# Optimization experiments

Hardware: AMD Instinct MI355X
Metric: run time of the kernel (lower is better)

## Reference

```python
import jax, jax.numpy as jnp
import numpy as np

B, S, D, H, K = 2, 2048, 1024, 16, 16


def setup_inputs() -> dict:
    key = jax.random.key(0)
    ks = jax.random.split(key, 8)
    s = 0.02
    def w(k, shape):
        return s * jax.random.normal(k, shape, jnp.float32)
    return {
        "x": jax.random.normal(ks[0], (B, S, D), jnp.float32),
        "Wq": w(ks[1], (D, D)), "bq": jnp.zeros((D,), jnp.float32),
        "Wk": w(ks[2], (D, D)), "bk": jnp.zeros((D,), jnp.float32),
        "Wv": w(ks[3], (D, D)), "bv": jnp.zeros((D,), jnp.float32),
        "Wo": w(ks[4], (D, D)), "bo": jnp.zeros((D,), jnp.float32),
        "Ws1": w(ks[5], (D, D // 2)), "bs1": jnp.zeros((D // 2,), jnp.float32),
        "Ws2": w(ks[6], (D // 2, 1)), "bs2": jnp.zeros((1,), jnp.float32),
    }


def reference(x, Wq, bq, Wk, bk, Wv, bv, Wo, bo, Ws1, bs1, Ws2, bs2):
    Bx, Sx, Dx = x.shape
    Dh = Dx // H
    # QKV projections -> [B, H, S, Dh]
    q = (x @ Wq + bq).reshape(Bx, Sx, H, Dh).transpose(0, 2, 1, 3)
    k = (x @ Wk + bk).reshape(Bx, Sx, H, Dh).transpose(0, 2, 1, 3)
    v = (x @ Wv + bv).reshape(Bx, Sx, H, Dh).transpose(0, 2, 1, 3)
    scores = jnp.einsum('bhqd,bhkd->bhqk', q, k) / np.float32(np.sqrt(Dh))
    # Lightning-indexer importance: [B, S]; identical across heads, so compute once.
    imp = jax.nn.sigmoid(jax.nn.relu(x @ Ws1 + bs1) @ Ws2 + bs2)[..., 0]
    _, idx = jax.lax.top_k(imp, K)  # [B, K]
    sel = jnp.zeros((Bx, Sx), bool).at[jnp.arange(Bx)[:, None], idx].set(True)
    # sparse mask: position (i, j) kept if row i OR column j is a top-k token
    m2 = sel[:, :, None] | sel[:, None, :]  # [B, S, S]
    masked = jnp.where(m2[:, None, :, :], scores, -jnp.inf)
    w = jax.nn.softmax(masked, axis=-1)
    att = jnp.einsum('bhqk,bhkd->bhqd', w, v).transpose(0, 2, 1, 3).reshape(Bx, Sx, Dx)
    return att @ Wo + bo
```

## Files before the change

kernel.cpp:

```cpp
#include <hip/hip_runtime.h>
#include <math.h>

constexpr int Bb = 2, Ss = 2048, Dd = 1024, Hh = 16, Kk = 16;

typedef __bf16 bf16x8 __attribute__((ext_vector_type(8)));
typedef __bf16 bf16x4 __attribute__((ext_vector_type(4)));
typedef float  f32x4  __attribute__((ext_vector_type(4)));

__device__ __forceinline__ void gld_lds16(const void* g, void* l) {
    __builtin_amdgcn_global_load_lds(
        (const __attribute__((address_space(1))) unsigned int*)g,
        (__attribute__((address_space(3))) unsigned int*)l, 16, 0, 0);
}

__device__ __forceinline__ unsigned fmap(float f) {
    unsigned u = __float_as_uint(f);
    return (u & 0x80000000u) ? ~u : (u | 0x80000000u);
}
__device__ __forceinline__ float funmap(unsigned u) {
    return (u & 0x80000000u) ? __uint_as_float(u ^ 0x80000000u) : __uint_as_float(~u);
}

__global__ void __launch_bounds__(256) gemm_qkv_ind(
    const __bf16* __restrict__ xb, const __bf16* __restrict__ xlo,
    const __bf16* __restrict__ WqT, const __bf16* __restrict__ WkT,
    const __bf16* __restrict__ WvT,
    const float* __restrict__ bq, const float* __restrict__ bk,
    const float* __restrict__ bv,
    __bf16* __restrict__ qb, __bf16* __restrict__ kb, __bf16* __restrict__ vb,
    const __bf16* __restrict__ W1Th, const __bf16* __restrict__ W1Tl,
    const float* __restrict__ bs1, const float* __restrict__ Ws2,
    float* __restrict__ imp)
{
    __shared__ __bf16 sm[16384];

    const int bid  = blockIdx.x;
    const int z    = bid & 3;
    const int rid  = bid >> 2;
    const int bxi  = rid & 7;
    const int bm   = (rid >> 3) * 128;
    const int t    = threadIdx.x;
    const int wave = t >> 6;
    const int lane = t & 63;
    const int fr   = lane & 15;
    const int fq   = lane >> 4;
    const int K    = Dd;

    if (z < 3) {
        const __bf16* BT  = (z == 0) ? WqT : (z == 1) ? WkT : WvT;
        const float* bias = (z == 0) ? bq  : (z == 1) ? bk  : bv;
        __bf16*      C    = (z == 0) ? qb  : (z == 1) ? kb  : vb;
        __bf16* As = sm;
        __bf16* Bs = sm + 8192;

        const int bn = bxi * 128;
        const int wm = (wave & 1) * 64;
        const int wn = (wave >> 1) * 64;

        f32x4 acc[4][4] = {};

        for (int k0 = 0; k0 < K; k0 += 64) {
            #pragma unroll
            for (int l = 0; l < 4; ++l) {
                int c = l * 256 + t;
                int row = c >> 3, seg = (c & 7) ^ (row & 7);
                gld_lds16(xb + (size_t)(bm + row) * K + k0 + seg * 8,
                          As + (size_t)(l * 256 + wave * 64) * 8);
                gld_lds16(BT + (size_t)(bn + row) * K + k0 + seg * 8,
                          Bs + (size_t)(l * 256 + wave * 64) * 8);
            }
            __syncthreads();

            #pragma unroll
            for (int s = 0; s < 2; ++s) {
                bf16x8 af[4], bf[4];
                #pragma unroll
                for (int i = 0; i < 4; ++i) {
                    int row = wm + i * 16 + fr;
                    af[i] = *(const bf16x8*)(As + row * 64 + (((s * 4 + fq) ^ (row & 7)) * 8));
                }
                #pragma unroll
                for (int j = 0; j < 4; ++j) {
                    int row = wn + j * 16 + fr;
                    bf[j] = *(const bf16x8*)(Bs + row * 64 + (((s * 4 + fq) ^ (row & 7)) * 8));
                }
                #pragma unroll
                for (int i = 0; i < 4; ++i)
                    #pragma unroll
                    for (int j = 0; j < 4; ++j)
                        acc[i][j] = __builtin_amdgcn_mfma_f32_16x16x32_bf16(af[i], bf[j], acc[i][j], 0, 0, 0);
            }
            __syncthreads();
        }

        const int cr = (lane >> 4) * 4;
        const int cc = lane & 15;
        #pragma unroll
        for (int j = 0; j < 4; ++j) {
            int col = bn + wn + j * 16 + cc;
            float bb = bias[col];
            #pragma unroll
            for (int i = 0; i < 4; ++i) {
                #pragma unroll
                for (int r = 0; r < 4; ++r)
                    C[(size_t)(bm + wm + i * 16 + cr + r) * Dd + col] =
                        (__bf16)(acc[i][j][r] + bb);
            }
        }
    } else {
        __bf16* Ah = sm;
        __bf16* Al = sm + 4096;
        __bf16* Bh = sm + 8192;
        __bf16* Bl = sm + 10240;

        const int bn = bxi * 64;
        const int wm = (wave & 1) * 64;
        const int wn = (wave >> 1) * 32;

        f32x4 acc[4][2] = {};

        for (int k0 = 0; k0 < K; k0 += 32) {
            #pragma unroll
            for (int l = 0; l < 2; ++l) {
                int c = l * 256 + t;
                int row = c >> 2, seg = (c & 3) ^ (row & 3);
                size_t goff = (size_t)(bm + row) * K + k0 + seg * 8;
                gld_lds16(xb  + goff, Ah + (size_t)(l * 256 + wave * 64) * 8);
                gld_lds16(xlo + goff, Al + (size_t)(l * 256 + wave * 64) * 8);
            }
            {
                int c = t;
                int row = c >> 2, seg = (c & 3) ^ (row & 3);
                size_t goff = (size_t)(bn + row) * K + k0 + seg * 8;
                gld_lds16(W1Th + goff, Bh + (size_t)(wave * 64) * 8);
                gld_lds16(W1Tl + goff, Bl + (size_t)(wave * 64) * 8);
            }
            __syncthreads();

            bf16x8 ah[4], al[4], bh[2], bl[2];
            #pragma unroll
            for (int i = 0; i < 4; ++i) {
                int row = wm + i * 16 + fr;
                int off = row * 32 + ((fq ^ (row & 3)) * 8);
                ah[i] = *(const bf16x8*)(Ah + off);
                al[i] = *(const bf16x8*)(Al + off);
            }
            #pragma unroll
            for (int j = 0; j < 2; ++j) {
                int row = wn + j * 16 + fr;
                int off = row * 32 + ((fq ^ (row & 3)) * 8);
                bh[j] = *(const bf16x8*)(Bh + off);
                bl[j] = *(const bf16x8*)(Bl + off);
            }
            #pragma unroll
            for (int i = 0; i < 4; ++i)
                #pragma unroll
                for (int j = 0; j < 2; ++j) {
                    acc[i][j] = __builtin_amdgcn_mfma_f32_16x16x32_bf16(al[i], bh[j], acc[i][j], 0, 0, 0);
                    acc[i][j] = __builtin_amdgcn_mfma_f32_16x16x32_bf16(ah[i], bl[j], acc[i][j], 0, 0, 0);
                    acc[i][j] = __builtin_amdgcn_mfma_f32_16x16x32_bf16(ah[i], bh[j], acc[i][j], 0, 0, 0);
                }
            __syncthreads();
        }

        const int cr = (lane >> 4) * 4;
        const int cc = lane & 15;
        float bb[2], w2[2];
        #pragma unroll
        for (int j = 0; j < 2; ++j) {
            int col = bn + wn + j * 16 + cc;
            bb[j] = bs1[col];
            w2[j] = Ws2[col];
        }
        #pragma unroll
        for (int i = 0; i < 4; ++i) {
            #pragma unroll
            for (int r = 0; r < 4; ++r) {
                float vsum = fmaxf(acc[i][0][r] + bb[0], 0.f) * w2[0]
                           + fmaxf(acc[i][1][r] + bb[1], 0.f) * w2[1];
                #pragma unroll
                for (int off = 8; off > 0; off >>= 1)
                    vsum += __shfl_xor(vsum, off, 16);
                if (cc == 0)
                    atomicAdd(imp + (bm + wm + i * 16 + cr + r), vsum);
            }
        }
    }
}

__global__ void __launch_bounds__(256) gemm_out(
    const __bf16* __restrict__ A, const __bf16* __restrict__ BT,
    const float* __restrict__ bias, float* __restrict__ C, int M, int N, int K)
{
    __shared__ __bf16 As[64 * 64];
    __shared__ __bf16 Bs[128 * 64];

    const int t    = threadIdx.x;
    const int wave = t >> 6;
    const int lane = t & 63;
    const int bm   = blockIdx.y * 64;
    const int bn   = blockIdx.x * 128;
    const int wm   = (wave & 1) * 32;
    const int wn   = (wave >> 1) * 64;
    const int fr   = lane & 15;
    const int fq   = lane >> 4;

    f32x4 acc[2][4] = {};

    for (int k0 = 0; k0 < K; k0 += 64) {
        #pragma unroll
        for (int l = 0; l < 2; ++l) {
            int c = l * 256 + t;
            int row = c >> 3, seg = (c & 7) ^ (row & 7);
            gld_lds16(A + (size_t)(bm + row) * K + k0 + seg * 8,
                      As + (size_t)(l * 256 + wave * 64) * 8);
        }
        #pragma unroll
        for (int l = 0; l < 4; ++l) {
            int c = l * 256 + t;
            int row = c >> 3, seg = (c & 7) ^ (row & 7);
            gld_lds16(BT + (size_t)(bn + row) * K + k0 + seg * 8,
                      Bs + (size_t)(l * 256 + wave * 64) * 8);
        }
        __syncthreads();

        #pragma unroll
        for (int s = 0; s < 2; ++s) {
            bf16x8 af[2], bf[4];
            #pragma unroll
            for (int i = 0; i < 2; ++i) {
                int row = wm + i * 16 + fr;
                af[i] = *(const bf16x8*)(As + row * 64 + (((s * 4 + fq) ^ (row & 7)) * 8));
            }
            #pragma unroll
            for (int j = 0; j < 4; ++j) {
                int row = wn + j * 16 + fr;
                bf[j] = *(const bf16x8*)(Bs + row * 64 + (((s * 4 + fq) ^ (row & 7)) * 8));
            }
            #pragma unroll
            for (int i = 0; i < 2; ++i)
                #pragma unroll
                for (int j = 0; j < 4; ++j)
                    acc[i][j] = __builtin_amdgcn_mfma_f32_16x16x32_bf16(af[i], bf[j], acc[i][j], 0, 0, 0);
        }
        __syncthreads();
    }

    const int cr = (lane >> 4) * 4;
    const int cc = lane & 15;
    #pragma unroll
    for (int j = 0; j < 4; ++j) {
        int col = bn + wn + j * 16 + cc;
        float bb = bias[col];
        #pragma unroll
        for (int i = 0; i < 2; ++i) {
            #pragma unroll
            for (int r = 0; r < 4; ++r)
                C[(size_t)(bm + wm + i * 16 + cr + r) * N + col] = acc[i][j][r] + bb;
        }
    }
}

__global__ void __launch_bounds__(256) prep_kernel(
    const float* __restrict__ x, __bf16* __restrict__ hi, __bf16* __restrict__ lo,
    float* __restrict__ imp, float* __restrict__ oacc,
    float* __restrict__ lsum, unsigned* __restrict__ macc,
    const float* __restrict__ W0, const float* __restrict__ W1,
    const float* __restrict__ W2, const float* __restrict__ W3,
    __bf16* __restrict__ T0, __bf16* __restrict__ T1,
    __bf16* __restrict__ T2, __bf16* __restrict__ T3,
    const float* __restrict__ Ws1, __bf16* __restrict__ Th, __bf16* __restrict__ Tl)
{
    __shared__ float tile[32][33];
    const int bid = blockIdx.x;

    if (bid < 4096) {
        int i = bid * 256 + threadIdx.x;
        if (i < Bb * Ss) imp[i] = 0.f;
        if (i < Bb * Hh * Kk * 64) oacc[i] = 0.f;
        if (i < Bb * Hh * Kk) { lsum[i] = 0.f; macc[i] = 0u; }
        float4 v = ((const float4*)x)[i];
        bf16x4 h = { (__bf16)v.x, (__bf16)v.y, (__bf16)v.z, (__bf16)v.w };
        bf16x4 l = { (__bf16)(v.x - (float)h[0]), (__bf16)(v.y - (float)h[1]),
                     (__bf16)(v.z - (float)h[2]), (__bf16)(v.w - (float)h[3]) };
        ((bf16x4*)hi)[i] = h;
        ((bf16x4*)lo)[i] = l;
        return;
    }

    int tid = bid - 4096;
    int z   = tid >> 10;
    int rem = tid & 1023;
    int n0  = (rem & 31) * 32;
    int k0  = (rem >> 5) * 32;
    int tx = threadIdx.x & 31, ty = threadIdx.x >> 5;

    if (z < 4) {
        const float* W = (z == 0) ? W0 : (z == 1) ? W1 : (z == 2) ? W2 : W3;
        __bf16*      T = (z == 0) ? T0 : (z == 1) ? T1 : (z == 2) ? T2 : T3;
        #pragma unroll
        for (int i = 0; i < 32; i += 8)
            tile[ty + i][tx] = W[(size_t)(k0 + ty + i) * 1024 + n0 + tx];
        __syncthreads();
        #pragma unroll
        for (int i = 0; i < 32; i += 8)
            T[(size_t)(n0 + ty + i) * 1024 + k0 + tx] = (__bf16)tile[tx][ty + i];
    } else {
        if (n0 >= 512) return;
        #pragma unroll
        for (int i = 0; i < 32; i += 8)
            tile[ty + i][tx] = Ws1[(size_t)(k0 + ty + i) * 512 + n0 + tx];
        __syncthreads();
        #pragma unroll
        for (int i = 0; i < 32; i += 8) {
            float v = tile[tx][ty + i];
            __bf16 h = (__bf16)v;
            Th[(size_t)(n0 + ty + i) * 1024 + k0 + tx] = h;
            Tl[(size_t)(n0 + ty + i) * 1024 + k0 + tx] = (__bf16)(v - (float)h);
        }
    }
}

__global__ void __launch_bounds__(256) topk_kernel(
    const float* __restrict__ imp, int* __restrict__ sel_idx)
{
    int b = blockIdx.x;
    int t = threadIdx.x;
    __shared__ float vals[Ss];
    __shared__ float sv[256];
    __shared__ int   si[256];

    for (int j = t; j < Ss; j += 256) vals[j] = imp[b * Ss + j];
    __syncthreads();

    for (int it = 0; it < Kk; ++it) {
        float best = -1e30f; int bidx = 0x7fffffff;
        for (int j = t; j < Ss; j += 256) {
            float v = vals[j];
            if (v > best || (v == best && j < bidx)) { best = v; bidx = j; }
        }
        sv[t] = best; si[t] = bidx;
        __syncthreads();
        for (int off = 128; off > 0; off >>= 1) {
            if (t < off) {
                float ov = sv[t + off]; int oi = si[t + off];
                if (ov > sv[t] || (ov == sv[t] && oi < si[t])) { sv[t] = ov; si[t] = oi; }
            }
            __syncthreads();
        }
        if (t == 0) {
            sel_idx[b * Kk + it] = si[0];
            vals[si[0]] = -1e30f;
        }
        __syncthreads();
    }
}

__global__ void __launch_bounds__(256) attn_sparse(
    const __bf16* __restrict__ q, const __bf16* __restrict__ k,
    const __bf16* __restrict__ v, const int* __restrict__ sel_idx,
    __bf16* __restrict__ att)
{
    const int b  = blockIdx.z;
    const int h  = blockIdx.y;
    const int q0 = blockIdx.x * 16;
    const int t  = threadIdx.x;

    __shared__ float KT[64][17];
    __shared__ float Vs[16][64];
    __shared__ float qsh[16][65];
    __shared__ float wsh[16][16];
    __shared__ int   sj[16];

    if (t < 16) sj[t] = sel_idx[b * Kk + t];
    __syncthreads();

    {
        int row = t >> 4, d0 = (t & 15) * 4;
        bf16x4 kv = *(const bf16x4*)(k + ((size_t)(b * Ss + sj[row])) * Dd + h * 64 + d0);
        bf16x4 vv = *(const bf16x4*)(v + ((size_t)(b * Ss + sj[row])) * Dd + h * 64 + d0);
        bf16x4 qv = *(const bf16x4*)(q + ((size_t)(b * Ss + q0 + row)) * Dd + h * 64 + d0);
        #pragma unroll
        for (int i = 0; i < 4; ++i) {
            KT[d0 + i][row]  = (float)kv[i];
            Vs[row][d0 + i]  = (float)vv[i];
            qsh[row][d0 + i] = (float)qv[i];
        }
    }
    __syncthreads();

    const int wave = t >> 6, lane = t & 63;
    const int ql = lane >> 4, j = lane & 15;
    const int qi = wave * 4 + ql;

    float s = 0.f;
    #pragma unroll
    for (int d = 0; d < 64; ++d) s = fmaf(qsh[qi][d], KT[d][j], s);
    s *= 0.125f;

    float m = s;
    #pragma unroll
    for (int off = 8; off > 0; off >>= 1) m = fmaxf(m, __shfl_xor(m, off, 16));
    float e = __expf(s - m);
    float sum = e;
    #pragma unroll
    for (int off = 8; off > 0; off >>= 1) sum += __shfl_xor(sum, off, 16);
    wsh[qi][j] = e / sum;

    #pragma unroll
    for (int q2 = 0; q2 < 4; ++q2) {
        int qq = wave * 4 + q2;
        float o = 0.f;
        #pragma unroll
        for (int jj = 0; jj < 16; ++jj)
            o = fmaf(wsh[qq][jj], Vs[jj][lane], o);
        att[((size_t)(b * Ss + q0 + qq)) * Dd + h * 64 + lane] = (__bf16)o;
    }
}

__global__ void __launch_bounds__(256) attn_dense_qk(
    const __bf16* __restrict__ q, const __bf16* __restrict__ k,
    const int* __restrict__ sel_idx, float* __restrict__ Sbuf,
    unsigned* __restrict__ macc)
{
    const int b  = blockIdx.z, h = blockIdx.y, j0 = blockIdx.x * 128;
    const int t  = threadIdx.x;

    __shared__ float Ks[128][65];
    __shared__ float Qs[16][65];

    #pragma unroll
    for (int l = 0; l < 4; ++l) {
        int c = t + 256 * l;
        int row = c >> 3, seg = c & 7;
        bf16x8 kv = *(const bf16x8*)(k + ((size_t)(b * Ss + j0 + row)) * Dd + h * 64 + seg * 8);
        #pragma unroll
        for (int e = 0; e < 8; ++e) Ks[row][seg * 8 + e] = (float)kv[e];
    }
    if (t < 128) {
        int row = t >> 3, seg = t & 7;
        int i = sel_idx[b * Kk + row];
        bf16x8 qv = *(const bf16x8*)(q + ((size_t)(b * Ss + i)) * Dd + h * 64 + seg * 8);
        #pragma unroll
        for (int e = 0; e < 8; ++e) Qs[row][seg * 8 + e] = (float)qv[e];
    }
    __syncthreads();

    const int qi = t >> 4, ks = t & 15;
    const int bhq = (b * Hh + h) * Kk + qi;
    float lmax = -1e30f;
    #pragma unroll
    for (int s8 = 0; s8 < 8; ++s8) {
        int j = ks + s8 * 16;
        float s = 0.f;
        #pragma unroll
        for (int d = 0; d < 64; ++d) s = fmaf(Qs[qi][d], Ks[j][d], s);
        s *= 0.125f;
        Sbuf[(size_t)bhq * Ss + j0 + j] = s;
        lmax = fmaxf(lmax, s);
    }
    #pragma unroll
    for (int off = 8; off > 0; off >>= 1) lmax = fmaxf(lmax, __shfl_xor(lmax, off, 16));
    if (ks == 0) atomicMax(macc + bhq, fmap(lmax));
}

__global__ void __launch_bounds__(256) attn_dense_pv(
    const __bf16* __restrict__ v, const float* __restrict__ Sbuf,
    const unsigned* __restrict__ macc, float* __restrict__ lsum,
    float* __restrict__ oacc)
{
    const int b  = blockIdx.z, h = blockIdx.y, j0 = blockIdx.x * 128;
    const int t  = threadIdx.x;

    __shared__ float Vs[128][64];
    __shared__ float Es[16][144];

    #pragma unroll
    for (int l = 0; l < 4; ++l) {
        int c = t + 256 * l;
        int row = c >> 3, seg = c & 7;
        bf16x8 vv = *(const bf16x8*)(v + ((size_t)(b * Ss + j0 + row)) * Dd + h * 64 + seg * 8);
        #pragma unroll
        for (int e = 0; e < 8; ++e) Vs[row][seg * 8 + e] = (float)vv[e];
    }

    const int qi = t >> 4, ks = t & 15;
    const int bhq = (b * Hh + h) * Kk + qi;
    const float mq = funmap(macc[bhq]);
    float psum = 0.f;
    #pragma unroll
    for (int s8 = 0; s8 < 8; ++s8) {
        int j = ks + s8 * 16;
        float e = __expf(Sbuf[(size_t)bhq * Ss + j0 + j] - mq);
        Es[qi][j] = e;
        psum += e;
    }
    #pragma unroll
    for (int off = 8; off > 0; off >>= 1) psum += __shfl_xor(psum, off, 16);
    if (ks == 0) atomicAdd(lsum + bhq, psum);
    __syncthreads();

    const int d = t & 63, qg = t >> 6;
    #pragma unroll
    for (int qq = 0; qq < 4; ++qq) {
        int qx = qg * 4 + qq;
        float o = 0.f;
        #pragma unroll 4
        for (int jj = 0; jj < 128; ++jj)
            o = fmaf(Es[qx][jj], Vs[jj][d], o);
        atomicAdd(oacc + (size_t)((b * Hh + h) * Kk + qx) * 64 + d, o);
    }
}

__global__ void __launch_bounds__(64) attn_dense_fin(
    const float* __restrict__ oacc, const float* __restrict__ lsum,
    const int* __restrict__ sel_idx, __bf16* __restrict__ att)
{
    int bid = blockIdx.x;
    int qi = bid & 15, h = (bid >> 4) & 15, b = bid >> 8;
    int bhq = (b * Hh + h) * Kk + qi;
    int i = sel_idx[b * Kk + qi];
    float val = oacc[(size_t)bhq * 64 + threadIdx.x] / lsum[bhq];
    att[((size_t)(b * Ss + i)) * Dd + h * 64 + threadIdx.x] = (__bf16)val;
}

extern "C" void kernel_launch(void* const* d_in, const int* in_sizes, int n_in,
                              void* d_out, int out_size, void* d_ws, size_t ws_size,
                              hipStream_t stream)
{
    const float* x   = (const float*)d_in[0];
    const float* Wq  = (const float*)d_in[1];
    const float* bq  = (const float*)d_in[2];
    const float* Wk  = (const float*)d_in[3];
    const float* bk  = (const float*)d_in[4];
    const float* Wv  = (const float*)d_in[5];
    const float* bv  = (const float*)d_in[6];
    const float* Wo  = (const float*)d_in[7];
    const float* bo  = (const float*)d_in[8];
    const float* Ws1 = (const float*)d_in[9];
    const float* bs1 = (const float*)d_in[10];
    const float* Ws2 = (const float*)d_in[11];
    float* out = (float*)d_out;

    const size_t MSD = (size_t)Bb * Ss * Dd;
    const int M = Bb * Ss;

    char* p = (char*)d_ws;
    __bf16* qb  = (__bf16*)p; p += MSD * sizeof(__bf16);
    __bf16* kb  = (__bf16*)p; p += MSD * sizeof(__bf16);
    __bf16* vb  = (__bf16*)p; p += MSD * sizeof(__bf16);
    __bf16* att = (__bf16*)p; p += MSD * sizeof(__bf16);
    __bf16* xb  = (__bf16*)p; p += MSD * sizeof(__bf16);
    __bf16* xlo = (__bf16*)p; p += MSD * sizeof(__bf16);
    __bf16* WqT = (__bf16*)p; p += (size_t)Dd * Dd * sizeof(__bf16);
    __bf16* WkT = (__bf16*)p; p += (size_t)Dd * Dd * sizeof(__bf16);
    __bf16* WvT = (__bf16*)p; p += (size_t)Dd * Dd * sizeof(__bf16);
    __bf16* WoT = (__bf16*)p; p += (size_t)Dd * Dd * sizeof(__bf16);
    __bf16* W1Th = (__bf16*)p; p += (size_t)512 * Dd * sizeof(__bf16);
    __bf16* W1Tl = (__bf16*)p; p += (size_t)512 * Dd * sizeof(__bf16);
    float* imp  = (float*)p; p += (size_t)Bb * Ss * sizeof(float);
    int* sel_idx = (int*)p; p += (size_t)Bb * Kk * sizeof(int);
    float* oacc = (float*)p; p += (size_t)Bb * Hh * Kk * 64 * sizeof(float);
    float* lsum = (float*)p; p += (size_t)Bb * Hh * Kk * sizeof(float);
    unsigned* macc = (unsigned*)p; p += (size_t)Bb * Hh * Kk * sizeof(unsigned);
    float* Sbuf = (float*)xlo;

    prep_kernel<<<dim3(4096 + 5120), 256, 0, stream>>>(
        x, xb, xlo, imp, oacc, lsum, macc,
        Wq, Wk, Wv, Wo, WqT, WkT, WvT, WoT, Ws1, W1Th, W1Tl);
    gemm_qkv_ind<<<dim3(1024), 256, 0, stream>>>(
        xb, xlo, WqT, WkT, WvT, bq, bk, bv, qb, kb, vb,
        W1Th, W1Tl, bs1, Ws2, imp);
    topk_kernel<<<dim3(Bb), 256, 0, stream>>>(imp, sel_idx);
    attn_sparse<<<dim3(Ss / 16, Hh, Bb), 256, 0, stream>>>(qb, kb, vb, sel_idx, att);
    attn_dense_qk<<<dim3(Ss / 128, Hh, Bb), 256, 0, stream>>>(qb, kb, sel_idx, Sbuf, macc);
    attn_dense_pv<<<dim3(Ss / 128, Hh, Bb), 256, 0, stream>>>(vb, Sbuf, macc, lsum, oacc);
    attn_dense_fin<<<dim3(Bb * Hh * Kk), 64, 0, stream>>>(oacc, lsum, sel_idx, att);
    gemm_out<<<dim3(8, 64), 256, 0, stream>>>(att, WoT, bo, out, M, Dd, Dd);
}
```

Baseline: 260.8 us.

## Score indexer in plain bf16, then rescore near-threshold candidates exactly in fp32

Drops the three-term bf16 split (hi/lo) emulation of fp32 for the indexer GEMM and computes it with single bf16 MFMAs, merged into one uniform 128x128 tiled GEMM with the QKV projections (concatenated WqkvT layout, 896 blocks). To keep top-k selection accurate, a candidate kernel collects the top 16 plus any token within a fixed margin of the 16th score (up to 64), rescoring them in full fp32 before a final wave-level top-k. This removes the xlo/W1Tl conversions and two-thirds of the indexer MFMA work, at the cost of two extra small launches and a risk of wrong selection if more than 64 candidates fall within the margin or if bf16 error exceeds DELTA.

```diff
diff --git a/kernel.cpp b/kernel.cpp
--- a/kernel.cpp
+++ b/kernel.cpp
@@ -2,6 +2,7 @@
 #include <math.h>
 
 constexpr int Bb = 2, Ss = 2048, Dd = 1024, Hh = 16, Kk = 16;
+constexpr float DELTA = 0.02f;
 
 typedef __bf16 bf16x8 __attribute__((ext_vector_type(8)));
 typedef __bf16 bf16x4 __attribute__((ext_vector_type(4)));
@@ -22,82 +23,78 @@
 }
 
 __global__ void __launch_bounds__(256) gemm_qkv_ind(
-    const __bf16* __restrict__ xb, const __bf16* __restrict__ xlo,
-    const __bf16* __restrict__ WqT, const __bf16* __restrict__ WkT,
-    const __bf16* __restrict__ WvT,
+    const __bf16* __restrict__ xb, const __bf16* __restrict__ WqkvT,
+    const __bf16* __restrict__ W1Th,
     const float* __restrict__ bq, const float* __restrict__ bk,
     const float* __restrict__ bv,
     __bf16* __restrict__ qb, __bf16* __restrict__ kb, __bf16* __restrict__ vb,
-    const __bf16* __restrict__ W1Th, const __bf16* __restrict__ W1Tl,
     const float* __restrict__ bs1, const float* __restrict__ Ws2,
     float* __restrict__ imp)
 {
-    __shared__ __bf16 sm[16384];
+    __shared__ __bf16 As[128 * 32];
+    __shared__ __bf16 Bs[128 * 32];
 
     const int bid  = blockIdx.x;
-    const int z    = bid & 3;
-    const int rid  = bid >> 2;
-    const int bxi  = rid & 7;
-    const int bm   = (rid >> 3) * 128;
+    const int cb   = bid % 28;
+    const int bm   = (bid / 28) * 128;
     const int t    = threadIdx.x;
     const int wave = t >> 6;
     const int lane = t & 63;
     const int fr   = lane & 15;
     const int fq   = lane >> 4;
     const int K    = Dd;
-
-    if (z < 3) {
-        const __bf16* BT  = (z == 0) ? WqT : (z == 1) ? WkT : WvT;
-        const float* bias = (z == 0) ? bq  : (z == 1) ? bk  : bv;
-        __bf16*      C    = (z == 0) ? qb  : (z == 1) ? kb  : vb;
-        __bf16* As = sm;
-        __bf16* Bs = sm + 8192;
-
-        const int bn = bxi * 128;
-        const int wm = (wave & 1) * 64;
-        const int wn = (wave >> 1) * 64;
-
-        f32x4 acc[4][4] = {};
-
-        for (int k0 = 0; k0 < K; k0 += 64) {
-            #pragma unroll
-            for (int l = 0; l < 4; ++l) {
-                int c = l * 256 + t;
-                int row = c >> 3, seg = (c & 7) ^ (row & 7);
-                gld_lds16(xb + (size_t)(bm + row) * K + k0 + seg * 8,
-                          As + (size_t)(l * 256 + wave * 64) * 8);
-                gld_lds16(BT + (size_t)(bn + row) * K + k0 + seg * 8,
-                          Bs + (size_t)(l * 256 + wave * 64) * 8);
-            }
-            __syncthreads();
-
-            #pragma unroll
-            for (int s = 0; s < 2; ++s) {
-                bf16x8 af[4], bf[4];
-                #pragma unroll
-                for (int i = 0; i < 4; ++i) {
-                    int row = wm + i * 16 + fr;
-                    af[i] = *(const bf16x8*)(As + row * 64 + (((s * 4 + fq) ^ (row & 7)) * 8));
-                }
-                #pragma unroll
-                for (int j = 0; j < 4; ++j) {
-                    int row = wn + j * 16 + fr;
-                    bf[j] = *(const bf16x8*)(Bs + row * 64 + (((s * 4 + fq) ^ (row & 7)) * 8));
-                }
-                #pragma unroll
-                for (int i = 0; i < 4; ++i)
-                    #pragma unroll
-                    for (int j = 0; j < 4; ++j)
-                        acc[i][j] = __builtin_amdgcn_mfma_f32_16x16x32_bf16(af[i], bf[j], acc[i][j], 0, 0, 0);
-            }
-            __syncthreads();
-        }
-
-        const int cr = (lane >> 4) * 4;
-        const int cc = lane & 15;
+    const bool ind = (cb >= 24);
+
+    const __bf16* BT = ind ? (W1Th + (size_t)(cb - 24) * 128 * 1024)
+                           : (WqkvT + (size_t)cb * 128 * 1024);
+
+    const int wm = (wave & 1) * 64;
+    const int wn = (wave >> 1) * 64;
+
+    f32x4 acc[4][4] = {};
+
+    for (int k0 = 0; k0 < K; k0 += 32) {
+        #pragma unroll
+        for (int l = 0; l < 2; ++l) {
+            int c = l * 256 + t;
+            int row = c >> 2, seg = (c & 3) ^ (row & 3);
+            gld_lds16(xb + (size_t)(bm + row) * K + k0 + seg * 8,
+                      As + (size_t)(l * 256 + wave * 64) * 8);
+            gld_lds16(BT + (size_t)row * K + k0 + seg * 8,
+                      Bs + (size_t)(l * 256 + wave * 64) * 8);
+        }
+        __syncthreads();
+
+        bf16x8 af[4], bf[4];
+        #pragma unroll
+        for (int i = 0; i < 4; ++i) {
+            int row = wm + i * 16 + fr;
+            af[i] = *(const bf16x8*)(As + row * 32 + ((fq ^ (row & 3)) * 8));
+        }
         #pragma unroll
         for (int j = 0; j < 4; ++j) {
-            int col = bn + wn + j * 16 + cc;
+            int row = wn + j * 16 + fr;
+            bf[j] = *(const bf16x8*)(Bs + row * 32 + ((fq ^ (row & 3)) * 8));
+        }
+        #pragma unroll
+        for (int i = 0; i < 4; ++i)
+            #pragma unroll
+            for (int j = 0; j < 4; ++j)
+                acc[i][j] = __builtin_amdgcn_mfma_f32_16x16x32_bf16(af[i], bf[j], acc[i][j], 0, 0, 0);
+        __syncthreads();
+    }
+
+    const int cr = (lane >> 4) * 4;
+    const int cc = lane & 15;
+
+    if (!ind) {
+        const int zone = cb >> 3;
+        const int cl0  = cb * 128 - zone * 1024;
+        const float* bias = (zone == 0) ? bq : (zone == 1) ? bk : bv;
+        __bf16*      C    = (zone == 0) ? qb : (zone == 1) ? kb : vb;
+        #pragma unroll
+        for (int j = 0; j < 4; ++j) {
+            int col = cl0 + wn + j * 16 + cc;
             float bb = bias[col];
             #pragma unroll
             for (int i = 0; i < 4; ++i) {
@@ -108,67 +105,11 @@
             }
         }
     } else {
-        __bf16* Ah = sm;
-        __bf16* Al = sm + 4096;
-        __bf16* Bh = sm + 8192;
-        __bf16* Bl = sm + 10240;
-
-        const int bn = bxi * 64;
-        const int wm = (wave & 1) * 64;
-        const int wn = (wave >> 1) * 32;
-
-        f32x4 acc[4][2] = {};
-
-        for (int k0 = 0; k0 < K; k0 += 32) {
-            #pragma unroll
-            for (int l = 0; l < 2; ++l) {
-                int c = l * 256 + t;
-                int row = c >> 2, seg = (c & 3) ^ (row & 3);
-                size_t goff = (size_t)(bm + row) * K + k0 + seg * 8;
-                gld_lds16(xb  + goff, Ah + (size_t)(l * 256 + wave * 64) * 8);
-                gld_lds16(xlo + goff, Al + (size_t)(l * 256 + wave * 64) * 8);
-            }
-            {
-                int c = t;
-                int row = c >> 2, seg = (c & 3) ^ (row & 3);
-                size_t goff = (size_t)(bn + row) * K + k0 + seg * 8;
-                gld_lds16(W1Th + goff, Bh + (size_t)(wave * 64) * 8);
-                gld_lds16(W1Tl + goff, Bl + (size_t)(wave * 64) * 8);
-            }
-            __syncthreads();
-
-            bf16x8 ah[4], al[4], bh[2], bl[2];
-            #pragma unroll
-            for (int i = 0; i < 4; ++i) {
-                int row = wm + i * 16 + fr;
-                int off = row * 32 + ((fq ^ (row & 3)) * 8);
-                ah[i] = *(const bf16x8*)(Ah + off);
-                al[i] = *(const bf16x8*)(Al + off);
-            }
-            #pragma unroll
-            for (int j = 0; j < 2; ++j) {
-                int row = wn + j * 16 + fr;
-                int off = row * 32 + ((fq ^ (row & 3)) * 8);
-                bh[j] = *(const bf16x8*)(Bh + off);
-                bl[j] = *(const bf16x8*)(Bl + off);
-            }
-            #pragma unroll
-            for (int i = 0; i < 4; ++i)
-                #pragma unroll
-                for (int j = 0; j < 2; ++j) {
-                    acc[i][j] = __builtin_amdgcn_mfma_f32_16x16x32_bf16(al[i], bh[j], acc[i][j], 0, 0, 0);
-                    acc[i][j] = __builtin_amdgcn_mfma_f32_16x16x32_bf16(ah[i], bl[j], acc[i][j], 0, 0, 0);
-                    acc[i][j] = __builtin_amdgcn_mfma_f32_16x16x32_bf16(ah[i], bh[j], acc[i][j], 0, 0, 0);
-                }
-            __syncthreads();
-        }
-
-        const int cr = (lane >> 4) * 4;
-        const int cc = lane & 15;
-        float bb[2], w2[2];
-        #pragma unroll
-        for (int j = 0; j < 2; ++j) {
-            int col = bn + wn + j * 16 + cc;
+        const int hc0 = (cb - 24) * 128;
+        float bb[4], w2[4];
+        #pragma unroll
+        for (int j = 0; j < 4; ++j) {
+            int col = hc0 + wn + j * 16 + cc;
             bb[j] = bs1[col];
             w2[j] = Ws2[col];
         }
@@ -176,8 +117,10 @@
         for (int i = 0; i < 4; ++i) {
             #pragma unroll
             for (int r = 0; r < 4; ++r) {
-                float vsum = fmaxf(acc[i][0][r] + bb[0], 0.f) * w2[0]
-                           + fmaxf(acc[i][1][r] + bb[1], 0.f) * w2[1];
+                float vsum = 0.f;
+                #pragma unroll
+                for (int j = 0; j < 4; ++j)
+                    vsum += fmaxf(acc[i][j][r] + bb[j], 0.f) * w2[j];
                 #pragma unroll
                 for (int off = 8; off > 0; off >>= 1)
                     vsum += __shfl_xor(vsum, off, 16);
@@ -262,14 +205,14 @@
 }
 
 __global__ void __launch_bounds__(256) prep_kernel(
-    const float* __restrict__ x, __bf16* __restrict__ hi, __bf16* __restrict__ lo,
+    const float* __restrict__ x, __bf16* __restrict__ xb,
     float* __restrict__ imp, float* __restrict__ oacc,
     float* __restrict__ lsum, unsigned* __restrict__ macc,
+    int* __restrict__ ccount,
     const float* __restrict__ W0, const float* __restrict__ W1,
     const float* __restrict__ W2, const float* __restrict__ W3,
-    __bf16* __restrict__ T0, __bf16* __restrict__ T1,
-    __bf16* __restrict__ T2, __bf16* __restrict__ T3,
-    const float* __restrict__ Ws1, __bf16* __restrict__ Th, __bf16* __restrict__ Tl)
+    __bf16* __restrict__ WqkvT, __bf16* __restrict__ WoT,
+    const float* __restrict__ Ws1, __bf16* __restrict__ Th)
 {
     __shared__ float tile[32][33];
     const int bid = blockIdx.x;
@@ -279,12 +222,10 @@
         if (i < Bb * Ss) imp[i] = 0.f;
         if (i < Bb * Hh * Kk * 64) oacc[i] = 0.f;
         if (i < Bb * Hh * Kk) { lsum[i] = 0.f; macc[i] = 0u; }
+        if (i < Bb) ccount[i] = 0;
         float4 v = ((const float4*)x)[i];
         bf16x4 h = { (__bf16)v.x, (__bf16)v.y, (__bf16)v.z, (__bf16)v.w };
-        bf16x4 l = { (__bf16)(v.x - (float)h[0]), (__bf16)(v.y - (float)h[1]),
-                     (__bf16)(v.z - (float)h[2]), (__bf16)(v.w - (float)h[3]) };
-        ((bf16x4*)hi)[i] = h;
-        ((bf16x4*)lo)[i] = l;
+        ((bf16x4*)xb)[i] = h;
         return;
     }
 
@@ -297,7 +238,7 @@
 
     if (z < 4) {
         const float* W = (z == 0) ? W0 : (z == 1) ? W1 : (z == 2) ? W2 : W3;
-        __bf16*      T = (z == 0) ? T0 : (z == 1) ? T1 : (z == 2) ? T2 : T3;
+        __bf16*      T = (z < 3) ? (WqkvT + (size_t)z * 1024 * 1024) : WoT;
         #pragma unroll
         for (int i = 0; i < 32; i += 8)
             tile[ty + i][tx] = W[(size_t)(k0 + ty + i) * 1024 + n0 + tx];
@@ -312,23 +253,22 @@
             tile[ty + i][tx] = Ws1[(size_t)(k0 + ty + i) * 512 + n0 + tx];
         __syncthreads();
         #pragma unroll
-        for (int i = 0; i < 32; i += 8) {
-            float v = tile[tx][ty + i];
-            __bf16 h = (__bf16)v;
-            Th[(size_t)(n0 + ty + i) * 1024 + k0 + tx] = h;
-            Tl[(size_t)(n0 + ty + i) * 1024 + k0 + tx] = (__bf16)(v - (float)h);
-        }
-    }
-}
-
-__global__ void __launch_bounds__(256) topk_kernel(
-    const float* __restrict__ imp, int* __restrict__ sel_idx)
+        for (int i = 0; i < 32; i += 8)
+            Th[(size_t)(n0 + ty + i) * 1024 + k0 + tx] = (__bf16)tile[tx][ty + i];
+    }
+}
+
+__global__ void __launch_bounds__(256) topk_cand(
+    const float* __restrict__ imp, int* __restrict__ cand_idx,
+    int* __restrict__ ccount)
 {
     int b = blockIdx.x;
     int t = threadIdx.x;
     __shared__ float vals[Ss];
     __shared__ float sv[256];
     __shared__ int   si[256];
+    __shared__ float thr_s;
+    __shared__ int   cnt_s;
 
     for (int j = t; j < Ss; j += 256) vals[j] = imp[b * Ss + j];
     __syncthreads();
@@ -349,10 +289,79 @@
             __syncthreads();
         }
         if (t == 0) {
-            sel_idx[b * Kk + it] = si[0];
+            cand_idx[b * 64 + it] = si[0];
             vals[si[0]] = -1e30f;
-        }
-        __syncthreads();
+            if (it == Kk - 1) { thr_s = sv[0] - DELTA; cnt_s = Kk; }
+        }
+        __syncthreads();
+    }
+
+    float thr = thr_s;
+    for (int j = t; j < Ss; j += 256) {
+        if (vals[j] > thr) {
+            int p = atomicAdd(&cnt_s, 1);
+            if (p < 64) cand_idx[b * 64 + p] = j;
+        }
+    }
+    __syncthreads();
+    if (t == 0) ccount[b] = min(cnt_s, 64);
+}
+
+__global__ void __launch_bounds__(256) rescore(
+    const float* __restrict__ x, const float* __restrict__ Ws1,
+    const float* __restrict__ bs1, const float* __restrict__ Ws2,
+    const int* __restrict__ cand_idx, const int* __restrict__ ccount,
+    float* __restrict__ candz)
+{
+    const int c = blockIdx.x, b = blockIdx.y;
+    if (c >= ccount[b]) return;
+    const int row = cand_idx[b * 64 + c];
+    const int t = threadIdx.x;
+
+    __shared__ float xs[1024];
+    __shared__ float red[256];
+
+    ((float4*)xs)[t] = ((const float4*)(x + ((size_t)(b * Ss + row)) * Dd))[t];
+    __syncthreads();
+
+    const int c0 = t, c1 = t + 256;
+    float h0 = 0.f, h1 = 0.f;
+    #pragma unroll 4
+    for (int kk = 0; kk < 1024; ++kk) {
+        float xv = xs[kk];
+        h0 = fmaf(xv, Ws1[(size_t)kk * 512 + c0], h0);
+        h1 = fmaf(xv, Ws1[(size_t)kk * 512 + c1], h1);
+    }
+    float zp = fmaxf(h0 + bs1[c0], 0.f) * Ws2[c0]
+             + fmaxf(h1 + bs1[c1], 0.f) * Ws2[c1];
+    red[t] = zp;
+    __syncthreads();
+    for (int off = 128; off > 0; off >>= 1) {
+        if (t < off) red[t] += red[t + off];
+        __syncthreads();
+    }
+    if (t == 0) candz[b * 64 + c] = red[0];
+}
+
+__global__ void __launch_bounds__(64) select_k(
+    const float* __restrict__ candz, const int* __restrict__ cand_idx,
+    const int* __restrict__ ccount, int* __restrict__ sel_idx)
+{
+    const int b = blockIdx.x, t = threadIdx.x;
+    const int cnt = ccount[b];
+    float val = (t < cnt) ? candz[b * 64 + t] : -1e30f;
+    int   row = (t < cnt) ? cand_idx[b * 64 + t] : 0x7fffffff;
+
+    for (int it = 0; it < Kk; ++it) {
+        float bv = val; int br = row;
+        #pragma unroll
+        for (int off = 1; off < 64; off <<= 1) {
+            float ov = __shfl_xor(bv, off, 64);
+            int   orw = __shfl_xor(br, off, 64);
+            if (ov > bv || (ov == bv && orw < br)) { bv = ov; br = orw; }
+        }
+        if (row == br) val = -1e30f;
+        if (t == 0) sel_idx[b * Kk + it] = br;
     }
 }
 
@@ -551,27 +560,28 @@
     __bf16* vb  = (__bf16*)p; p += MSD * sizeof(__bf16);
     __bf16* att = (__bf16*)p; p += MSD * sizeof(__bf16);
     __bf16* xb  = (__bf16*)p; p += MSD * sizeof(__bf16);
-    __bf16* xlo = (__bf16*)p; p += MSD * sizeof(__bf16);
-    __bf16* WqT = (__bf16*)p; p += (size_t)Dd * Dd * sizeof(__bf16);
-    __bf16* WkT = (__bf16*)p; p += (size_t)Dd * Dd * sizeof(__bf16);
-    __bf16* WvT = (__bf16*)p; p += (size_t)Dd * Dd * sizeof(__bf16);
-    __bf16* WoT = (__bf16*)p; p += (size_t)Dd * Dd * sizeof(__bf16);
-    __bf16* W1Th = (__bf16*)p; p += (size_t)512 * Dd * sizeof(__bf16);
-    __bf16* W1Tl = (__bf16*)p; p += (size_t)512 * Dd * sizeof(__bf16);
+    float* Sbuf = (float*)p; p += (size_t)Bb * Hh * Kk * Ss * sizeof(float);
+    __bf16* WqkvT = (__bf16*)p; p += (size_t)3 * Dd * Dd * sizeof(__bf16);
+    __bf16* WoT   = (__bf16*)p; p += (size_t)Dd * Dd * sizeof(__bf16);
+    __bf16* W1Th  = (__bf16*)p; p += (size_t)512 * Dd * sizeof(__bf16);
     float* imp  = (float*)p; p += (size_t)Bb * Ss * sizeof(float);
     int* sel_idx = (int*)p; p += (size_t)Bb * Kk * sizeof(int);
     float* oacc = (float*)p; p += (size_t)Bb * Hh * Kk * 64 * sizeof(float);
     float* lsum = (float*)p; p += (size_t)Bb * Hh * Kk * sizeof(float);
     unsigned* macc = (unsigned*)p; p += (size_t)Bb * Hh * Kk * sizeof(unsigned);
-    float* Sbuf = (float*)xlo;
+    int* ccount   = (int*)p; p += Bb * sizeof(int);
+    int* cand_idx = (int*)p; p += (size_t)Bb * 64 * sizeof(int);
+    float* candz  = (float*)p; p += (size_t)Bb * 64 * sizeof(float);
 
     prep_kernel<<<dim3(4096 + 5120), 256, 0, stream>>>(
-        x, xb, xlo, imp, oacc, lsum, macc,
-        Wq, Wk, Wv, Wo, WqT, WkT, WvT, WoT, Ws1, W1Th, W1Tl);
-    gemm_qkv_ind<<<dim3(1024), 256, 0, stream>>>(
-        xb, xlo, WqT, WkT, WvT, bq, bk, bv, qb, kb, vb,
-        W1Th, W1Tl, bs1, Ws2, imp);
-    topk_kernel<<<dim3(Bb), 256, 0, stream>>>(imp, sel_idx);
+        x, xb, imp, oacc, lsum, macc, ccount,
+        Wq, Wk, Wv, Wo, WqkvT, WoT, Ws1, W1Th);
+    gemm_qkv_ind<<<dim3(896), 256, 0, stream>>>(
+        xb, WqkvT, W1Th, bq, bk, bv, qb, kb, vb, bs1, Ws2, imp);
+    topk_cand<<<dim3(Bb), 256, 0, stream>>>(imp, cand_idx, ccount);
+    rescore<<<dim3(64, Bb), 256, 0, stream>>>(
+        x, Ws1, bs1, Ws2, cand_idx, ccount, candz);
+    select_k<<<dim3(Bb), 64, 0, stream>>>(candz, cand_idx, ccount, sel_idx);
     attn_sparse<<<dim3(Ss / 16, Hh, Bb), 256, 0, stream>>>(qb, kb, vb, sel_idx, att);
     attn_dense_qk<<<dim3(Ss / 128, Hh, Bb), 256, 0, stream>>>(qb, kb, sel_idx, Sbuf, macc);
     attn_dense_pv<<<dim3(Ss / 128, Hh, Bb), 256, 0, stream>>>(vb, Sbuf, macc, lsum, oacc);
```

Result: slower. 324.0 us (+24.3%).
